# Performance work log

Hardware: AMD Instinct MI355X
Metric: run time of the kernel (lower is better)

The kernel has to match this reference:

```python
import jax, jax.numpy as jnp
import numpy as np

H = 12  # hidden size hard-coded in the module

def _lstm_cell(x, h, c, w_ih, w_hh, b_ih, b_hh):
    # PyTorch LSTMCell gate order: input, forget, cell(g), output
    gates = x @ w_ih.T + b_ih + h @ w_hh.T + b_hh  # [B, 4H]
    i, f, g, o = jnp.split(gates, 4, axis=-1)
    c_new = jax.nn.sigmoid(f) * c + jax.nn.sigmoid(i) * jnp.tanh(g)
    h_new = jax.nn.sigmoid(o) * jnp.tanh(c_new)
    return h_new, c_new

def setup_inputs() -> dict:
    key = jax.random.key(0)
    ks = jax.random.split(key, 12)
    B, T = 8192, 1024
    s = 1.0 / np.sqrt(H)  # torch LSTMCell/Linear init scale
    u = lambda k, shape: jax.random.uniform(k, shape, jnp.float32, -s, s)
    return {
        "input": jax.random.normal(ks[0], (B, T), jnp.float32),
        "future": 64,
        "w_ih1": u(ks[1], (4 * H, 1)),
        "w_hh1": u(ks[2], (4 * H, H)),
        "b_ih1": u(ks[3], (4 * H,)),
        "b_hh1": u(ks[4], (4 * H,)),
        "w_ih2": u(ks[5], (4 * H, H)),
        "w_hh2": u(ks[6], (4 * H, H)),
        "b_ih2": u(ks[7], (4 * H,)),
        "b_hh2": u(ks[8], (4 * H,)),
        "w_lin": u(ks[9], (1, H)),
        "b_lin": u(ks[10], (1,)),
    }

def reference(input, future, w_ih1, w_hh1, b_ih1, b_hh1,
              w_ih2, w_hh2, b_ih2, b_hh2, w_lin, b_lin):
    B, T = input.shape
    xs = input.T[:, :, None]  # [T, B, 1]
    if future > 0:
        # Faithful to the original: free-running steps keep feeding the LAST input chunk
        last = jnp.broadcast_to(xs[-1], (future, B, 1))
        xs = jnp.concatenate([xs, last], axis=0)  # [T+future, B, 1]

    def step(carry, x_t):
        h1, c1, h2, c2 = carry
        h1, c1 = _lstm_cell(x_t, h1, c1, w_ih1, w_hh1, b_ih1, b_hh1)
        h2, c2 = _lstm_cell(h1, h2, c2, w_ih2, w_hh2, b_ih2, b_hh2)
        y = h2 @ w_lin.T + b_lin  # [B, 1]
        return (h1, c1, h2, c2), y[:, 0]

    z = jnp.zeros((B, H), input.dtype)
    _, ys = jax.lax.scan(step, (z, z, z, z), xs)  # ys: [T+future, B]
    return ys.T  # [B, T+future] == stack(outputs,1).squeeze(2)
```

## Files before the change

### kernel.cpp

```cpp
#include <hip/hip_runtime.h>


typedef _Float16 v8h  __attribute__((ext_vector_type(8)));
typedef _Float16 v4h  __attribute__((ext_vector_type(4)));
typedef float    v4f  __attribute__((ext_vector_type(4)));

constexpr int T   = 1024;
constexpr int FUT = 64;
constexpr int TT  = T + FUT;
constexpr int B   = 8192;

static __device__ __forceinline__ float fexp2(float x){ return __builtin_amdgcn_exp2f(x); }
static __device__ __forceinline__ float frcp (float x){ return __builtin_amdgcn_rcpf(x); }

__global__ __launch_bounds__(256) void lstm_quad_kernel(
    const float* __restrict__ input,
    const float* __restrict__ w_ih1, const float* __restrict__ w_hh1,
    const float* __restrict__ b_ih1, const float* __restrict__ b_hh1,
    const float* __restrict__ w_ih2, const float* __restrict__ w_hh2,
    const float* __restrict__ b_ih2, const float* __restrict__ b_hh2,
    const float* __restrict__ w_lin, const float* __restrict__ b_lin,
    float* __restrict__ out)
{
  const int tid  = threadIdx.x;
  const int wid  = tid >> 6;
  const int ch   = wid >> 1;
  const int cw   = wid & 1;
  const int lane = tid & 63;
  const int g    = lane >> 4;
  const int n    = lane & 15;
  const int e0   = blockIdx.x * 32 + ch * 16;

  const float L2E = 1.4426950408889634f;
  const float sc[4] = { -L2E, -L2E, 2.0f * L2E, -L2E };
  const float TWO_L2E = 2.885390081777927f;

  v8h Aw[3]; v4f Cw[3];
  float wix[3][4];
  float wl[3] = {0,0,0};
  {
    const int q = n & 3;
    #pragma unroll
    for (int c = 0; c < 3; ++c) {
      const int v   = 4 * c + (n >> 2);
      const int row = q * 12 + v;
      v8h a = {0,0,0,0,0,0,0,0};
      if (cw == 0) {
        #pragma unroll
        for (int j = 0; j < 3; ++j)
          a[j] = (_Float16)(sc[q] * w_hh1[row * 12 + (4 * j + g)]);
      } else {
        #pragma unroll
        for (int j = 0; j < 3; ++j) {
          const int u = 4 * j + g;
          a[j]     = (_Float16)(sc[q] * w_ih2[row * 12 + u]);
          a[j + 4] = (_Float16)(sc[q] * w_hh2[row * 12 + u]);
        }
      }
      Aw[c] = a;
    }
    #pragma unroll
    for (int c = 0; c < 3; ++c) {
      const int v = 4 * c + g;
      #pragma unroll
      for (int r = 0; r < 4; ++r) {
        if (cw == 0) {
          Cw[c][r]  = sc[r] * (b_ih1[r * 12 + v] + b_hh1[r * 12 + v]);
          wix[c][r] = sc[r] * w_ih1[r * 12 + v];
        } else {
          Cw[c][r]  = sc[r] * (b_ih2[r * 12 + v] + b_hh2[r * 12 + v]);
          wix[c][r] = 0.0f;
        }
      }
      if (cw == 1) wl[c] = w_lin[v];
    }
  }
  const float blin = b_lin[0];

  __shared__ v4h  fifo[2][16][64];
  __shared__ float yP[2][16][4][16];

  float csw[3] = {0,0,0};
  v8h  Bw = {0,0,0,0,0,0,0,0};

  const float* xrow = input + (size_t)(e0 + n) * T;
  float*       yrow = out   + (size_t)(e0 + n) * TT;
  const float  xl   = xrow[T - 1];

  auto act3 = [&](const float (&G)[3][4], float (&h)[3]) {
    float Ai[3], Af[3], Eg[3], Ao[3];
    #pragma unroll
    for (int c = 0; c < 3; ++c) Ai[c] = fexp2(G[c][0]);
    #pragma unroll
    for (int c = 0; c < 3; ++c) Af[c] = fexp2(G[c][1]);
    #pragma unroll
    for (int c = 0; c < 3; ++c) Eg[c] = fexp2(G[c][2]);
    #pragma unroll
    for (int c = 0; c < 3; ++c) Ao[c] = fexp2(G[c][3]);
    float pfx[3], P[3], R[3], Nn[3], Ec[3], R2[3];
    #pragma unroll
    for (int c = 0; c < 3; ++c) { pfx[c] = 1.0f + Af[c]; P[c] = (1.0f + Ai[c]) * (1.0f + Eg[c]); }
    #pragma unroll
    for (int c = 0; c < 3; ++c) R[c]  = frcp(P[c] * pfx[c]);
    #pragma unroll
    for (int c = 0; c < 3; ++c) Nn[c] = fmaf(csw[c], P[c], (Eg[c] - 1.0f) * pfx[c]);
    #pragma unroll
    for (int c = 0; c < 3; ++c) csw[c] = Nn[c] * R[c];
    #pragma unroll
    for (int c = 0; c < 3; ++c) Ec[c] = fexp2(TWO_L2E * csw[c]);
    #pragma unroll
    for (int c = 0; c < 3; ++c) R2[c] = frcp((1.0f + Ao[c]) * (1.0f + Ec[c]));
    #pragma unroll
    for (int c = 0; c < 3; ++c) h[c] = (Ec[c] - 1.0f) * R2[c];
  };

  auto stepA = [&](int t, float x) {
    v4f D0 = __builtin_amdgcn_mfma_f32_16x16x32_f16(Aw[0], Bw, Cw[0], 0, 0, 0);
    v4f D1 = __builtin_amdgcn_mfma_f32_16x16x32_f16(Aw[1], Bw, Cw[1], 0, 0, 0);
    v4f D2 = __builtin_amdgcn_mfma_f32_16x16x32_f16(Aw[2], Bw, Cw[2], 0, 0, 0);
    float G[3][4], h[3];
    #pragma unroll
    for (int r = 0; r < 4; ++r) G[0][r] = fmaf(wix[0][r], x, D0[r]);
    #pragma unroll
    for (int r = 0; r < 4; ++r) G[1][r] = fmaf(wix[1][r], x, D1[r]);
    #pragma unroll
    for (int r = 0; r < 4; ++r) G[2][r] = fmaf(wix[2][r], x, D2[r]);
    act3(G, h);
    v4h pk;
    pk[0] = (_Float16)h[0]; pk[1] = (_Float16)h[1];
    pk[2] = (_Float16)h[2]; pk[3] = (_Float16)0.0f;
    fifo[ch][t & 15][lane] = pk;
    Bw[0] = pk[0]; Bw[1] = pk[1]; Bw[2] = pk[2];
  };

  auto stepB = [&](v4h pf, int s) {
    Bw[0] = pf[0]; Bw[1] = pf[1]; Bw[2] = pf[2];
    v4f E0 = __builtin_amdgcn_mfma_f32_16x16x32_f16(Aw[0], Bw, Cw[0], 0, 0, 0);
    v4f E1 = __builtin_amdgcn_mfma_f32_16x16x32_f16(Aw[1], Bw, Cw[1], 0, 0, 0);
    v4f E2 = __builtin_amdgcn_mfma_f32_16x16x32_f16(Aw[2], Bw, Cw[2], 0, 0, 0);
    float G[3][4], h[3];
    #pragma unroll
    for (int r = 0; r < 4; ++r) G[0][r] = E0[r];
    #pragma unroll
    for (int r = 0; r < 4; ++r) G[1][r] = E1[r];
    #pragma unroll
    for (int r = 0; r < 4; ++r) G[2][r] = E2[r];
    act3(G, h);
    Bw[4] = (_Float16)h[0]; Bw[5] = (_Float16)h[1]; Bw[6] = (_Float16)h[2];
    float yp = h[0] * wl[0];
    yp = fmaf(h[1], wl[1], yp);
    yp = fmaf(h[2], wl[2], yp);
    yP[ch][s & 15][g][n] = yp;
  };

  auto flush = [&](int sbase) {
    const int tq = lane >> 4;
    float ys[4];
    #pragma unroll
    for (int ii = 0; ii < 4; ++ii) {
      const int j = 4 * tq + ii;
      ys[ii] = (yP[ch][j][0][n] + yP[ch][j][1][n])
             + (yP[ch][j][2][n] + yP[ch][j][3][n]) + blin;
    }
    *reinterpret_cast<float4*>(yrow + sbase + 4 * tq) =
        make_float4(ys[0], ys[1], ys[2], ys[3]);
  };

  float4 xc0 = make_float4(0,0,0,0), xc1 = xc0;
  if (cw == 0) {
    xc0 = *reinterpret_cast<const float4*>(xrow);
    xc1 = *reinterpret_cast<const float4*>(xrow + 4);
  }

  for (int kb = 0; kb <= TT; kb += 8) {
    if (cw == 0) {
      if (kb < TT) {
        float4 xn0, xn1;
        const int nb = kb + 8;
        if (nb < T) {
          xn0 = *reinterpret_cast<const float4*>(xrow + nb);
          xn1 = *reinterpret_cast<const float4*>(xrow + nb + 4);
        } else {
          xn0 = make_float4(xl, xl, xl, xl);
          xn1 = xn0;
        }
        stepA(kb + 0, xc0.x);
        stepA(kb + 1, xc0.y);
        stepA(kb + 2, xc0.z);
        stepA(kb + 3, xc0.w);
        stepA(kb + 4, xc1.x);
        stepA(kb + 5, xc1.y);
        stepA(kb + 6, xc1.z);
        stepA(kb + 7, xc1.w);
        xc0 = xn0; xc1 = xn1;
      }
    } else {
      if (kb >= 8) {
        const int s0 = kb - 8;
        v4h p0 = fifo[ch][(s0 + 0) & 15][lane];
        v4h p1 = fifo[ch][(s0 + 1) & 15][lane];
        v4h p2 = fifo[ch][(s0 + 2) & 15][lane];
        v4h p3 = fifo[ch][(s0 + 3) & 15][lane];
        v4h p4 = fifo[ch][(s0 + 4) & 15][lane];
        v4h p5 = fifo[ch][(s0 + 5) & 15][lane];
        v4h p6 = fifo[ch][(s0 + 6) & 15][lane];
        v4h p7 = fifo[ch][(s0 + 7) & 15][lane];
        stepB(p0, s0 + 0);
        stepB(p1, s0 + 1);
        stepB(p2, s0 + 2);
        stepB(p3, s0 + 3);
        stepB(p4, s0 + 4);
        stepB(p5, s0 + 5);
        stepB(p6, s0 + 6);
        stepB(p7, s0 + 7);
        if ((kb & 15) == 0) flush(kb - 16);
      }
    }
    __syncthreads();
  }
}

extern "C" void kernel_launch(void* const* d_in, const int* in_sizes, int n_in,
                              void* d_out, int out_size, void* d_ws, size_t ws_size,
                              hipStream_t stream) {
  const float* input = (const float*)d_in[0];
  const float* w_ih1 = (const float*)d_in[2];
  const float* w_hh1 = (const float*)d_in[3];
  const float* b_ih1 = (const float*)d_in[4];
  const float* b_hh1 = (const float*)d_in[5];
  const float* w_ih2 = (const float*)d_in[6];
  const float* w_hh2 = (const float*)d_in[7];
  const float* b_ih2 = (const float*)d_in[8];
  const float* b_hh2 = (const float*)d_in[9];
  const float* w_lin = (const float*)d_in[10];
  const float* b_lin = (const float*)d_in[11];
  float* out = (float*)d_out;

  dim3 grid(B / 32);
  dim3 block(256);
  hipLaunchKernelGGL(lstm_quad_kernel, grid, block, 0, stream,
                     input, w_ih1, w_hh1, b_ih1, b_hh1,
                     w_ih2, w_hh2, b_ih2, b_hh2, w_lin, b_lin, out);
}
```

Measured before the change: 357.0 us.

## Move layer-2 input projection into layer-1 warps and fold x into MFMA

Layer-1 warps now also compute the layer-2 input projection (W_ih2·h1 plus bias) with extra MFMAs and pass fp32 partial gate accumulators through shared memory. Layer-2 warps then need only the recurrent W_hh2 MFMA. The scalar x·w_ih1 FMAs are replaced by a split-fp16 hi/lo encoding of x placed in an unused K slot of the MFMA. The tanh scaling is folded into the cell-state representation, and __syncthreads is replaced by a raw lgkmcnt wait plus s_barrier. This rebalances the critical path between the two warp groups, at the cost of a larger shared FIFO (fp32 v4f ×3 instead of v4h) and more LDS traffic.

```diff
diff --git a/kernel.cpp b/kernel.cpp
--- a/kernel.cpp
+++ b/kernel.cpp
@@ -2,7 +2,6 @@
 
 
 typedef _Float16 v8h  __attribute__((ext_vector_type(8)));
-typedef _Float16 v4h  __attribute__((ext_vector_type(4)));
 typedef float    v4f  __attribute__((ext_vector_type(4)));
 
 constexpr int T   = 1024;
@@ -13,7 +12,11 @@
 static __device__ __forceinline__ float fexp2(float x){ return __builtin_amdgcn_exp2f(x); }
 static __device__ __forceinline__ float frcp (float x){ return __builtin_amdgcn_rcpf(x); }
 
-__global__ __launch_bounds__(256) void lstm_quad_kernel(
+static __device__ __forceinline__ void lgkm_barrier() {
+  asm volatile("s_waitcnt lgkmcnt(0)\n\ts_barrier" ::: "memory");
+}
+
+__global__ __launch_bounds__(256) void lstm_r18_kernel(
     const float* __restrict__ input,
     const float* __restrict__ w_ih1, const float* __restrict__ w_hh1,
     const float* __restrict__ b_ih1, const float* __restrict__ b_hh1,
@@ -35,8 +38,10 @@
   const float sc[4] = { -L2E, -L2E, 2.0f * L2E, -L2E };
   const float TWO_L2E = 2.885390081777927f;
 
-  v8h Aw[3]; v4f Cw[3];
-  float wix[3][4];
+  v8h Aw[3];
+  v8h A2h1[3];
+  v4f Cw[3];
+  v4f C2r[3];
   float wl[3] = {0,0,0};
   {
     const int q = n & 3;
@@ -44,20 +49,26 @@
     for (int c = 0; c < 3; ++c) {
       const int v   = 4 * c + (n >> 2);
       const int row = q * 12 + v;
-      v8h a = {0,0,0,0,0,0,0,0};
+      v8h a = {0,0,0,0,0,0,0,0}, a2 = {0,0,0,0,0,0,0,0};
       if (cw == 0) {
-        #pragma unroll
-        for (int j = 0; j < 3; ++j)
-          a[j] = (_Float16)(sc[q] * w_hh1[row * 12 + (4 * j + g)]);
-      } else {
         #pragma unroll
         for (int j = 0; j < 3; ++j) {
           const int u = 4 * j + g;
-          a[j]     = (_Float16)(sc[q] * w_ih2[row * 12 + u]);
-          a[j + 4] = (_Float16)(sc[q] * w_hh2[row * 12 + u]);
+          a[j]  = (_Float16)(sc[q] * w_hh1[row * 12 + u]);
+          a2[j] = (_Float16)(sc[q] * w_ih2[row * 12 + u]);
         }
-      }
-      Aw[c] = a;
+        const float wfull = sc[q] * w_ih1[row];
+        const _Float16 whi = (_Float16)wfull;
+        const _Float16 wlo = (_Float16)(wfull - (float)whi);
+        a[3] = (g == 0 || g == 1) ? whi : (g == 2 ? wlo : (_Float16)0);
+      } else {
+        #pragma unroll
+        for (int j = 0; j < 3; ++j)
+          a2[j + 4] = (_Float16)(sc[q] * w_hh2[row * 12 + (4 * j + g)]);
+        a = a2;
+      }
+      if (cw == 0) { Aw[c] = a; A2h1[c] = a2; }
+      else         { Aw[c] = a; }
     }
     #pragma unroll
     for (int c = 0; c < 3; ++c) {
@@ -66,10 +77,9 @@
       for (int r = 0; r < 4; ++r) {
         if (cw == 0) {
           Cw[c][r]  = sc[r] * (b_ih1[r * 12 + v] + b_hh1[r * 12 + v]);
-          wix[c][r] = sc[r] * w_ih1[r * 12 + v];
+          C2r[c][r] = sc[r] * (b_ih2[r * 12 + v] + b_hh2[r * 12 + v]);
         } else {
-          Cw[c][r]  = sc[r] * (b_ih2[r * 12 + v] + b_hh2[r * 12 + v]);
-          wix[c][r] = 0.0f;
+          Cw[c][r]  = 0.0f; C2r[c][r] = 0.0f;
         }
       }
       if (cw == 1) wl[c] = w_lin[v];
@@ -77,7 +87,7 @@
   }
   const float blin = b_lin[0];
 
-  __shared__ v4h  fifo[2][16][64];
+  __shared__ v4f  fifoD[2][16][3][64];
   __shared__ float yP[2][16][4][16];
 
   float csw[3] = {0,0,0};
@@ -97,47 +107,55 @@
     for (int c = 0; c < 3; ++c) Eg[c] = fexp2(G[c][2]);
     #pragma unroll
     for (int c = 0; c < 3; ++c) Ao[c] = fexp2(G[c][3]);
-    float pfx[3], P[3], R[3], Nn[3], Ec[3], R2[3];
+    float pfx[3], P[3], R[3], T2[3], Nn[3], Ec[3], R2[3];
     #pragma unroll
     for (int c = 0; c < 3; ++c) { pfx[c] = 1.0f + Af[c]; P[c] = (1.0f + Ai[c]) * (1.0f + Eg[c]); }
     #pragma unroll
     for (int c = 0; c < 3; ++c) R[c]  = frcp(P[c] * pfx[c]);
     #pragma unroll
-    for (int c = 0; c < 3; ++c) Nn[c] = fmaf(csw[c], P[c], (Eg[c] - 1.0f) * pfx[c]);
+    for (int c = 0; c < 3; ++c) T2[c] = fmaf(Eg[c], TWO_L2E, -TWO_L2E) * pfx[c];
+    #pragma unroll
+    for (int c = 0; c < 3; ++c) Nn[c] = fmaf(csw[c], P[c], T2[c]);
     #pragma unroll
     for (int c = 0; c < 3; ++c) csw[c] = Nn[c] * R[c];
     #pragma unroll
-    for (int c = 0; c < 3; ++c) Ec[c] = fexp2(TWO_L2E * csw[c]);
+    for (int c = 0; c < 3; ++c) Ec[c] = fexp2(csw[c]);
     #pragma unroll
     for (int c = 0; c < 3; ++c) R2[c] = frcp((1.0f + Ao[c]) * (1.0f + Ec[c]));
     #pragma unroll
     for (int c = 0; c < 3; ++c) h[c] = (Ec[c] - 1.0f) * R2[c];
   };
 
-  auto stepA = [&](int t, float x) {
+  auto stepA = [&](int t, float xs) {
+    const _Float16 xh = (_Float16)xs;
+    const _Float16 xo = (_Float16)(xs - (float)xh);
+    Bw[3] = (g == 1) ? xo : ((g == 3) ? (_Float16)0 : xh);
+
     v4f D0 = __builtin_amdgcn_mfma_f32_16x16x32_f16(Aw[0], Bw, Cw[0], 0, 0, 0);
     v4f D1 = __builtin_amdgcn_mfma_f32_16x16x32_f16(Aw[1], Bw, Cw[1], 0, 0, 0);
     v4f D2 = __builtin_amdgcn_mfma_f32_16x16x32_f16(Aw[2], Bw, Cw[2], 0, 0, 0);
     float G[3][4], h[3];
     #pragma unroll
-    for (int r = 0; r < 4; ++r) G[0][r] = fmaf(wix[0][r], x, D0[r]);
-    #pragma unroll
-    for (int r = 0; r < 4; ++r) G[1][r] = fmaf(wix[1][r], x, D1[r]);
-    #pragma unroll
-    for (int r = 0; r < 4; ++r) G[2][r] = fmaf(wix[2][r], x, D2[r]);
+    for (int r = 0; r < 4; ++r) G[0][r] = D0[r];
+    #pragma unroll
+    for (int r = 0; r < 4; ++r) G[1][r] = D1[r];
+    #pragma unroll
+    for (int r = 0; r < 4; ++r) G[2][r] = D2[r];
     act3(G, h);
-    v4h pk;
-    pk[0] = (_Float16)h[0]; pk[1] = (_Float16)h[1];
-    pk[2] = (_Float16)h[2]; pk[3] = (_Float16)0.0f;
-    fifo[ch][t & 15][lane] = pk;
-    Bw[0] = pk[0]; Bw[1] = pk[1]; Bw[2] = pk[2];
-  };
-
-  auto stepB = [&](v4h pf, int s) {
-    Bw[0] = pf[0]; Bw[1] = pf[1]; Bw[2] = pf[2];
-    v4f E0 = __builtin_amdgcn_mfma_f32_16x16x32_f16(Aw[0], Bw, Cw[0], 0, 0, 0);
-    v4f E1 = __builtin_amdgcn_mfma_f32_16x16x32_f16(Aw[1], Bw, Cw[1], 0, 0, 0);
-    v4f E2 = __builtin_amdgcn_mfma_f32_16x16x32_f16(Aw[2], Bw, Cw[2], 0, 0, 0);
+    Bw[0] = (_Float16)h[0]; Bw[1] = (_Float16)h[1]; Bw[2] = (_Float16)h[2];
+
+    v4f P0 = __builtin_amdgcn_mfma_f32_16x16x32_f16(A2h1[0], Bw, C2r[0], 0, 0, 0);
+    v4f P1 = __builtin_amdgcn_mfma_f32_16x16x32_f16(A2h1[1], Bw, C2r[1], 0, 0, 0);
+    v4f P2 = __builtin_amdgcn_mfma_f32_16x16x32_f16(A2h1[2], Bw, C2r[2], 0, 0, 0);
+    fifoD[ch][t & 15][0][lane] = P0;
+    fifoD[ch][t & 15][1][lane] = P1;
+    fifoD[ch][t & 15][2][lane] = P2;
+  };
+
+  auto stepB = [&](const v4f (&pd)[3], int s) {
+    v4f E0 = __builtin_amdgcn_mfma_f32_16x16x32_f16(Aw[0], Bw, pd[0], 0, 0, 0);
+    v4f E1 = __builtin_amdgcn_mfma_f32_16x16x32_f16(Aw[1], Bw, pd[1], 0, 0, 0);
+    v4f E2 = __builtin_amdgcn_mfma_f32_16x16x32_f16(Aw[2], Bw, pd[2], 0, 0, 0);
     float G[3][4], h[3];
     #pragma unroll
     for (int r = 0; r < 4; ++r) G[0][r] = E0[r];
@@ -181,8 +199,7 @@
           xn0 = *reinterpret_cast<const float4*>(xrow + nb);
           xn1 = *reinterpret_cast<const float4*>(xrow + nb + 4);
         } else {
-          xn0 = make_float4(xl, xl, xl, xl);
-          xn1 = xn0;
+          xn0 = make_float4(xl, xl, xl, xl); xn1 = xn0;
         }
         stepA(kb + 0, xc0.x);
         stepA(kb + 1, xc0.y);
@@ -197,26 +214,25 @@
     } else {
       if (kb >= 8) {
         const int s0 = kb - 8;
-        v4h p0 = fifo[ch][(s0 + 0) & 15][lane];
-        v4h p1 = fifo[ch][(s0 + 1) & 15][lane];
-        v4h p2 = fifo[ch][(s0 + 2) & 15][lane];
-        v4h p3 = fifo[ch][(s0 + 3) & 15][lane];
-        v4h p4 = fifo[ch][(s0 + 4) & 15][lane];
-        v4h p5 = fifo[ch][(s0 + 5) & 15][lane];
-        v4h p6 = fifo[ch][(s0 + 6) & 15][lane];
-        v4h p7 = fifo[ch][(s0 + 7) & 15][lane];
-        stepB(p0, s0 + 0);
-        stepB(p1, s0 + 1);
-        stepB(p2, s0 + 2);
-        stepB(p3, s0 + 3);
-        stepB(p4, s0 + 4);
-        stepB(p5, s0 + 5);
-        stepB(p6, s0 + 6);
-        stepB(p7, s0 + 7);
+        v4f pd[4][3];
+        #pragma unroll
+        for (int s = 0; s < 4; ++s)
+          #pragma unroll
+          for (int c = 0; c < 3; ++c)
+            pd[s][c] = fifoD[ch][(s0 + s) & 15][c][lane];
+        #pragma unroll
+        for (int s = 0; s < 4; ++s) stepB(pd[s], s0 + s);
+        #pragma unroll
+        for (int s = 0; s < 4; ++s)
+          #pragma unroll
+          for (int c = 0; c < 3; ++c)
+            pd[s][c] = fifoD[ch][(s0 + 4 + s) & 15][c][lane];
+        #pragma unroll
+        for (int s = 0; s < 4; ++s) stepB(pd[s], s0 + 4 + s);
         if ((kb & 15) == 0) flush(kb - 16);
       }
     }
-    __syncthreads();
+    lgkm_barrier();
   }
 }
 
@@ -238,7 +254,7 @@
 
   dim3 grid(B / 32);
   dim3 block(256);
-  hipLaunchKernelGGL(lstm_quad_kernel, grid, block, 0, stream,
+  hipLaunchKernelGGL(lstm_r18_kernel, grid, block, 0, stream,
                      input, w_ih1, w_hh1, b_ih1, b_hh1,
                      w_ih2, w_hh2, b_ih2, b_hh2, w_lin, b_lin, out);
 }
```

Result: slower. 401.4 us (+12.4%).
